# Kernel optimization log

Measured on AMD Instinct MI355X. Metric: run time of the kernel, lower is better.

## Reference

```python
import jax, jax.numpy as jnp
import numpy as np

PH, PW = 2, 2            # patch_size
SHUFFLE_PROB = 0.1       # shuffle_prob


def setup_inputs() -> dict:
    key = jax.random.key(0)
    x = jax.random.normal(key, (16, 64, 256, 256), dtype=jnp.float32)
    return {"x": x}


def reference(x):
    # Faithful vectorized PatchShuffle (training mode):
    #  - per-sample Bernoulli(shuffle_prob) decides whether that sample is shuffled
    #  - if shuffled, EVERY channel's EVERY (PH x PW) patch gets an independent
    #    random permutation of its pixels (torch calls randperm per (b, c, patch))
    B, C, H, W = x.shape
    Hp, Wp = H // PH, W // PW
    P = PH * PW

    key = jax.random.key(42)
    kmask, kperm = jax.random.split(key)

    # [B,C,H,W] -> [B,C,Hp,Wp,P]  (patch-major layout, pixels of a patch last)
    patches = (
        x.reshape(B, C, Hp, PH, Wp, PW)
        .transpose(0, 1, 2, 4, 3, 5)
        .reshape(B, C, Hp, Wp, P)
    )

    # Independent uniform permutation per (b, c, patch): argsort of iid uniforms.
    perm = jnp.argsort(jax.random.uniform(kperm, (B, C, Hp, Wp, P)), axis=-1)
    shuffled = jnp.take_along_axis(patches, perm, axis=-1)

    # back to [B,C,H,W]
    shuffled = (
        shuffled.reshape(B, C, Hp, Wp, PH, PW)
        .transpose(0, 1, 2, 4, 3, 5)
        .reshape(B, C, H, W)
    )

    # per-sample shuffle decision (torch.rand(1).item() < shuffle_prob)
    mask = jax.random.uniform(kmask, (B,)) < SHUFFLE_PROB
    return jnp.where(mask[:, None, None, None], shuffled, x)
```

## Files before the change

kernel.cpp:

```cpp
#include <hip/hip_runtime.h>
#include <cstdint>
#include <cstring>

#ifndef THREEFRY_PARTITIONABLE
#define THREEFRY_PARTITIONABLE 1
#endif

static constexpr int B_ = 16, C_ = 64, H_ = 256, W_ = 256;
static constexpr uint32_t NPATCH = (uint32_t)B_ * C_ * (H_ / 2) * (W_ / 2);
static constexpr uint32_t NBLOCK = 2048;
static constexpr uint32_t NCHUNK = NPATCH / 512;
static constexpr uint32_t NITER  = NCHUNK / NBLOCK;

__host__ __device__ __forceinline__ void tf2x32(uint32_t k0, uint32_t k1,
                                                uint32_t c0, uint32_t c1,
                                                uint32_t& o0, uint32_t& o1) {
  const uint32_t ks2 = k0 ^ k1 ^ 0x1BD11BDAu;
  uint32_t x0 = c0 + k0, x1 = c1 + k1;
#define TFR(r) { x0 += x1; x1 = (x1 << (r)) | (x1 >> (32 - (r))); x1 ^= x0; }
  TFR(13) TFR(15) TFR(26) TFR(6)
  x0 += k1;  x1 += ks2 + 1u;
  TFR(17) TFR(29) TFR(16) TFR(24)
  x0 += ks2; x1 += k0 + 2u;
  TFR(13) TFR(15) TFR(26) TFR(6)
  x0 += k0;  x1 += k1 + 3u;
  TFR(17) TFR(29) TFR(16) TFR(24)
  x0 += k1;  x1 += ks2 + 4u;
  TFR(13) TFR(15) TFR(26) TFR(6)
  x0 += ks2; x1 += k0 + 5u;
#undef TFR
  o0 = x0; o1 = x1;
}

__device__ __forceinline__ uint32_t perm_bits(uint32_t kp0, uint32_t kp1, uint32_t j) {
  uint32_t w0, w1;
#if THREEFRY_PARTITIONABLE
  tf2x32(kp0, kp1, 0u, j, w0, w1);
  return w0 ^ w1;
#else
  uint32_t lo = j & 0x01FFFFFFu;
  tf2x32(kp0, kp1, lo, lo + 0x02000000u, w0, w1);
  return (j < 0x02000000u) ? w0 : w1;
#endif
}

__device__ __forceinline__ void shuffle4(const float v[4], const uint32_t s[4], float o[4]) {
  int r0 = 0, r1 = 0, r2 = 0, r3 = 0;
  if (s[1] < s[0]) r0++; else r1++;
  if (s[2] < s[0]) r0++; else r2++;
  if (s[3] < s[0]) r0++; else r3++;
  if (s[2] < s[1]) r1++; else r2++;
  if (s[3] < s[1]) r1++; else r3++;
  if (s[3] < s[2]) r2++; else r3++;
  o[0] = (r0 == 0) ? v[0] : (r1 == 0) ? v[1] : (r2 == 0) ? v[2] : v[3];
  o[1] = (r0 == 1) ? v[0] : (r1 == 1) ? v[1] : (r2 == 1) ? v[2] : v[3];
  o[2] = (r0 == 2) ? v[0] : (r1 == 2) ? v[1] : (r2 == 2) ? v[2] : v[3];
  o[3] = (r0 == 3) ? v[0] : (r1 == 3) ? v[1] : (r2 == 3) ? v[2] : v[3];
}

__device__ __forceinline__ void shuffle_patch(uint32_t kp0, uint32_t kp1, uint32_t patch,
                                              float p0, float p1, float p2, float p3,
                                              float o[4]) {
  const uint32_t jbase = patch << 2;
  uint32_t s[4];
#pragma unroll
  for (int p = 0; p < 4; ++p) s[p] = perm_bits(kp0, kp1, jbase + (uint32_t)p) >> 9;
  const float v[4] = {p0, p1, p2, p3};
  shuffle4(v, s, o);
}

__device__ __forceinline__ void emit_chunk(float* __restrict__ out, uint32_t base,
                                           uint32_t gid, bool shuf,
                                           uint32_t kp0, uint32_t kp1,
                                           const float4& r0, const float4& r1) {
  float4* d0 = reinterpret_cast<float4*>(out + base);
  float4* d1 = reinterpret_cast<float4*>(out + base + W_);
  if (!shuf) { *d0 = r0; *d1 = r1; return; }
  float oA[4], oB[4];
  shuffle_patch(kp0, kp1, gid + 0u, r0.x, r0.y, r1.x, r1.y, oA);
  shuffle_patch(kp0, kp1, gid + 1u, r0.z, r0.w, r1.z, r1.w, oB);
  *d0 = make_float4(oA[0], oA[1], oB[0], oB[1]);
  *d1 = make_float4(oA[2], oA[3], oB[2], oB[3]);
}

__global__ __launch_bounds__(256, 8) void PatchShuffle_26869315404121_kernel(
    const float* __restrict__ x, float* __restrict__ out,
    uint32_t kp0, uint32_t kp1, uint32_t maskbits) {
  const uint32_t tid = threadIdx.x;
  const uint32_t bid = blockIdx.x;

#pragma unroll 1
  for (uint32_t it = 0; it < NITER; it += 2) {
    const uint32_t c0 = it * NBLOCK + bid;
    const uint32_t c1 = c0 + NBLOCK;
    const uint32_t g0 = c0 * 512u + tid * 2u;
    const uint32_t g1 = c1 * 512u + tid * 2u;
    const uint32_t b0 = (g0 >> 7) * 512u + (g0 & 127u) * 2u;
    const uint32_t b1 = (g1 >> 7) * 512u + (g1 & 127u) * 2u;

    const float4 r00 = *reinterpret_cast<const float4*>(x + b0);
    const float4 r01 = *reinterpret_cast<const float4*>(x + b0 + W_);
    const float4 r10 = *reinterpret_cast<const float4*>(x + b1);
    const float4 r11 = *reinterpret_cast<const float4*>(x + b1 + W_);

    emit_chunk(out, b0, g0, (maskbits >> it) & 1u, kp0, kp1, r00, r01);
    emit_chunk(out, b1, g1, (maskbits >> (it + 1u)) & 1u, kp0, kp1, r10, r11);
  }
}

extern "C" void kernel_launch(void* const* d_in, const int* in_sizes, int n_in,
                              void* d_out, int out_size, void* d_ws, size_t ws_size,
                              hipStream_t stream) {
  const float* x = (const float*)d_in[0];
  float* out = (float*)d_out;

  const uint32_t k0 = 0u, k1 = 42u;
  uint32_t km0, km1, kp0, kp1;
#if THREEFRY_PARTITIONABLE
  tf2x32(k0, k1, 0u, 0u, km0, km1);
  tf2x32(k0, k1, 0u, 1u, kp0, kp1);
#else
  {
    uint32_t a0, a1, b0v, b1v;
    tf2x32(k0, k1, 0u, 2u, a0, a1);
    tf2x32(k0, k1, 1u, 3u, b0v, b1v);
    km0 = a0; km1 = b0v;
    kp0 = a1; kp1 = b1v;
  }
#endif

  uint32_t maskbits = 0u;
  for (uint32_t s = 0; s < 16u; ++s) {
    uint32_t w0, w1, bits;
#if THREEFRY_PARTITIONABLE
    tf2x32(km0, km1, 0u, s, w0, w1);
    bits = w0 ^ w1;
#else
    uint32_t i = s & 7u;
    tf2x32(km0, km1, i, i + 8u, w0, w1);
    bits = (s < 8u) ? w0 : w1;
#endif
    uint32_t fb = (bits >> 9) | 0x3F800000u;
    float u;
    std::memcpy(&u, &fb, sizeof(u));
    u -= 1.0f;
    if (u < 0.1f) maskbits |= (1u << s);
  }

  PatchShuffle_26869315404121_kernel<<<NBLOCK, 256, 0, stream>>>(
      x, out, kp0, kp1, maskbits);
}
```

Before: 109.2 us.

## Copy unshuffled samples with memcpy, launch shuffle kernel only on masked samples

The per-sample Bernoulli mask is evaluated on the host, and contiguous runs of unshuffled samples are copied with device-to-device hipMemcpyAsync. A compact kernel, one block per 512-patch chunk, runs only over the shuffled samples, whose indices are packed into a 64-bit argument. This takes the per-element mask branch and the shuffle logic off the copy path for most samples. In exchange it may issue several memcpy operations plus a kernel launch per call, which adds launch overhead.

After: 112.7 us. +3.1%, slower.

```diff
diff --git a/kernel.cpp b/kernel.cpp
--- a/kernel.cpp
+++ b/kernel.cpp
@@ -7,10 +7,8 @@
 #endif
 
 static constexpr int B_ = 16, C_ = 64, H_ = 256, W_ = 256;
-static constexpr uint32_t NPATCH = (uint32_t)B_ * C_ * (H_ / 2) * (W_ / 2);
-static constexpr uint32_t NBLOCK = 2048;
-static constexpr uint32_t NCHUNK = NPATCH / 512;
-static constexpr uint32_t NITER  = NCHUNK / NBLOCK;
+static constexpr uint32_t CHW = (uint32_t)C_ * H_ * W_;
+static constexpr uint32_t BLOCKS_PER_SAMPLE = 2048;
 
 __host__ __device__ __forceinline__ void tf2x32(uint32_t k0, uint32_t k1,
                                                 uint32_t c0, uint32_t c1,
@@ -69,43 +67,29 @@
   shuffle4(v, s, o);
 }
 
-__device__ __forceinline__ void emit_chunk(float* __restrict__ out, uint32_t base,
-                                           uint32_t gid, bool shuf,
-                                           uint32_t kp0, uint32_t kp1,
-                                           const float4& r0, const float4& r1) {
+__global__ __launch_bounds__(256) void PatchShuffle_26869315404121_kernel(
+    const float* __restrict__ x, float* __restrict__ out,
+    uint32_t kp0, uint32_t kp1, uint64_t ids) {
+  const uint32_t bid    = blockIdx.x;
+  const uint32_t widx   = bid >> 11;
+  const uint32_t sample = (uint32_t)((ids >> (4u * widx)) & 15u);
+  const uint32_t chunk  = bid & (BLOCKS_PER_SAMPLE - 1u);
+  const uint32_t gid    = (sample << 20) | (chunk << 9) | (threadIdx.x << 1);
+
+  const uint32_t wp   = gid & 127u;
+  const uint32_t rest = gid >> 7;
+  const uint32_t base = rest * 512u + wp * 2u;
+
+  const float4 r0 = *reinterpret_cast<const float4*>(x + base);
+  const float4 r1 = *reinterpret_cast<const float4*>(x + base + W_);
   float4* d0 = reinterpret_cast<float4*>(out + base);
   float4* d1 = reinterpret_cast<float4*>(out + base + W_);
-  if (!shuf) { *d0 = r0; *d1 = r1; return; }
+
   float oA[4], oB[4];
   shuffle_patch(kp0, kp1, gid + 0u, r0.x, r0.y, r1.x, r1.y, oA);
   shuffle_patch(kp0, kp1, gid + 1u, r0.z, r0.w, r1.z, r1.w, oB);
   *d0 = make_float4(oA[0], oA[1], oB[0], oB[1]);
   *d1 = make_float4(oA[2], oA[3], oB[2], oB[3]);
-}
-
-__global__ __launch_bounds__(256, 8) void PatchShuffle_26869315404121_kernel(
-    const float* __restrict__ x, float* __restrict__ out,
-    uint32_t kp0, uint32_t kp1, uint32_t maskbits) {
-  const uint32_t tid = threadIdx.x;
-  const uint32_t bid = blockIdx.x;
-
-#pragma unroll 1
-  for (uint32_t it = 0; it < NITER; it += 2) {
-    const uint32_t c0 = it * NBLOCK + bid;
-    const uint32_t c1 = c0 + NBLOCK;
-    const uint32_t g0 = c0 * 512u + tid * 2u;
-    const uint32_t g1 = c1 * 512u + tid * 2u;
-    const uint32_t b0 = (g0 >> 7) * 512u + (g0 & 127u) * 2u;
-    const uint32_t b1 = (g1 >> 7) * 512u + (g1 & 127u) * 2u;
-
-    const float4 r00 = *reinterpret_cast<const float4*>(x + b0);
-    const float4 r01 = *reinterpret_cast<const float4*>(x + b0 + W_);
-    const float4 r10 = *reinterpret_cast<const float4*>(x + b1);
-    const float4 r11 = *reinterpret_cast<const float4*>(x + b1 + W_);
-
-    emit_chunk(out, b0, g0, (maskbits >> it) & 1u, kp0, kp1, r00, r01);
-    emit_chunk(out, b1, g1, (maskbits >> (it + 1u)) & 1u, kp0, kp1, r10, r11);
-  }
 }
 
 extern "C" void kernel_launch(void* const* d_in, const int* in_sizes, int n_in,
@@ -147,6 +131,25 @@
     if (u < 0.1f) maskbits |= (1u << s);
   }
 
-  PatchShuffle_26869315404121_kernel<<<NBLOCK, 256, 0, stream>>>(
-      x, out, kp0, kp1, maskbits);
+  uint64_t ids = 0;
+  uint32_t nshuf = 0;
+  for (uint32_t s = 0; s < 16u; ++s) {
+    if ((maskbits >> s) & 1u) { ids |= ((uint64_t)s) << (4u * nshuf); ++nshuf; }
+  }
+
+  uint32_t s = 0;
+  while (s < 16u) {
+    if ((maskbits >> s) & 1u) { ++s; continue; }
+    uint32_t e = s;
+    while (e < 16u && !((maskbits >> e) & 1u)) ++e;
+    const size_t off   = (size_t)s * CHW;
+    const size_t bytes = (size_t)(e - s) * CHW * sizeof(float);
+    hipMemcpyAsync(out + off, x + off, bytes, hipMemcpyDeviceToDevice, stream);
+    s = e;
+  }
+
+  if (nshuf > 0) {
+    PatchShuffle_26869315404121_kernel<<<nshuf * BLOCKS_PER_SAMPLE, 256, 0, stream>>>(
+        x, out, kp0, kp1, ids);
+  }
 }
```
